# Kernel optimization log

Measured on AMD Instinct MI355X. Metric: run time of the kernel, lower is better.

Reference implementation:

```python
import jax, jax.numpy as jnp
import numpy as np
from jax import lax

D, C, H, W = 4, 64, 64, 64
QK = 32  # q/k projection channels


def _conv3x3(x, w, b):
    # x: [D,C,H,W], w: [O,I,3,3] -> [D,O,H,W], SAME padding, stride 1
    y = lax.conv_general_dilated(x, w, window_strides=(1, 1), padding='SAME',
                                 dimension_numbers=('NCHW', 'OIHW', 'NCHW'))
    return y + b[None, :, None, None]


def setup_inputs() -> dict:
    key = jax.random.key(0)
    ks = jax.random.split(key, 6)
    x = jax.random.normal(ks[0], (D, C, H, W), dtype=jnp.float32)
    atten = jax.random.normal(ks[1], (D, H * W, H * W), dtype=jnp.float32)
    q_w = jax.random.normal(ks[2], (QK, C, 3, 3), dtype=jnp.float32) * 0.05
    q_b = jax.random.normal(ks[3], (QK,), dtype=jnp.float32) * 0.05
    k_w = jax.random.normal(ks[4], (QK, C, 3, 3), dtype=jnp.float32) * 0.05
    k_b = jax.random.normal(ks[5], (QK,), dtype=jnp.float32) * 0.05
    gamma = jnp.ones((1,), dtype=jnp.float32)
    return {"x": x, "atten": atten, "q_w": q_w, "q_b": q_b,
            "k_w": k_w, "k_b": k_b, "gamma": gamma}


def reference(x, atten, q_w, q_b, k_w, k_b, gamma):
    d, c, h, w = x.shape
    n = h * w
    q = _conv3x3(x, q_w, q_b).reshape(d, QK, n)   # [D,32,N]
    k = _conv3x3(x, k_w, k_b).reshape(d, QK, n)   # [D,32,N]
    v = x.reshape(d, c, n)                         # [D,C,N]
    # attention = softmax(q^T k), then softmax(attention + atten) -- double softmax
    attn = jax.nn.softmax(jnp.einsum('dcn,dcm->dnm', q, k), axis=-1)  # [D,N,N]
    attn = jax.nn.softmax(attn + atten, axis=-1)
    # out = v @ attn^T  -> [D,C,N]
    out = jnp.einsum('dcm,dnm->dcn', v, attn).reshape(d, c, h, w)
    return gamma * out + x
```

## Files before the change

kernel.cpp:

```cpp
#include <hip/hip_runtime.h>
#include <hip/hip_bf16.h>

typedef float  f32x4  __attribute__((ext_vector_type(4)));
typedef float  f32x4u __attribute__((ext_vector_type(4), aligned(4)));
typedef short  s16x4  __attribute__((ext_vector_type(4)));
typedef short  s16x8  __attribute__((ext_vector_type(8)));
typedef __bf16 bf16x8 __attribute__((ext_vector_type(8)));

#define N_PIX 4096

__device__ __forceinline__ unsigned short f2bf(float f) {
    __hip_bfloat16 h = __float2bfloat16(f);
    return *reinterpret_cast<unsigned short*>(&h);
}
__device__ __forceinline__ float bf2f(unsigned short u) {
    __hip_bfloat16 h;
    *reinterpret_cast<unsigned short*>(&h) = u;
    return __bfloat162float(h);
}

#if __has_builtin(__builtin_amdgcn_mfma_f32_16x16x16bf16_1k)
#define USE_K16 1
#else
#define USE_K16 0
#endif

__device__ __forceinline__ f32x4 mac_k32v(s16x8 a8, s16x8 b8, f32x4 c) {
#if USE_K16
    s16x4 alo = __builtin_shufflevector(a8, a8, 0, 1, 2, 3);
    s16x4 ahi = __builtin_shufflevector(a8, a8, 4, 5, 6, 7);
    s16x4 blo = __builtin_shufflevector(b8, b8, 0, 1, 2, 3);
    s16x4 bhi = __builtin_shufflevector(b8, b8, 4, 5, 6, 7);
    c = __builtin_amdgcn_mfma_f32_16x16x16bf16_1k(alo, blo, c, 0, 0, 0);
    c = __builtin_amdgcn_mfma_f32_16x16x16bf16_1k(ahi, bhi, c, 0, 0, 0);
#else
    c = __builtin_amdgcn_mfma_f32_16x16x32_bf16(__builtin_bit_cast(bf16x8, a8),
                                                __builtin_bit_cast(bf16x8, b8), c, 0, 0, 0);
#endif
    return c;
}

__global__ __launch_bounds__(256) void to_bf16_kernel(const float* __restrict__ x,
                                                      unsigned short* __restrict__ v_bf) {
    int i = blockIdx.x * 256 + threadIdx.x;
    f32x4 f = *(const f32x4*)(x + i * 4);
    s16x4 p;
    p[0] = (short)f2bf(f[0]); p[1] = (short)f2bf(f[1]);
    p[2] = (short)f2bf(f[2]); p[3] = (short)f2bf(f[3]);
    *(s16x4*)(v_bf + i * 4) = p;
}

__global__ __launch_bounds__(256) void pad_kernel(const float* __restrict__ x,
                                                  float* __restrict__ xp) {
    int i = blockIdx.x * 256 + threadIdx.x;
    int xx = i % 66;
    int t  = i / 66;
    int yy = t % 66;
    int cd = t / 66;
    float v = 0.f;
    if (xx >= 1 && xx <= 64 && yy >= 1 && yy <= 64)
        v = x[(size_t)cd * 4096 + (yy - 1) * 64 + (xx - 1)];
    xp[i] = v;
}

__global__ __launch_bounds__(256) void conv_qk_kernel(
    const float* __restrict__ xp,
    const float* __restrict__ q_w, const float* __restrict__ q_b,
    const float* __restrict__ k_w, const float* __restrict__ k_b,
    unsigned short* __restrict__ qTp_hi, unsigned short* __restrict__ qTp_lo,
    unsigned short* __restrict__ kTp_hi, unsigned short* __restrict__ kTp_lo) {
    int bid = blockIdx.x;
    int d    = bid & 3;
    int rest = bid >> 2;
    int o  = __builtin_amdgcn_readfirstlane(rest & 31);
    int yg = rest >> 5;
    int tid = threadIdx.x;
    int y   = yg * 4 + (tid >> 6);
    int col = tid & 63;
    const float* xc0 = xp + (size_t)d * (64 * 4356) + y * 66 + col;
    const float* wq = q_w + o * 576;
    const float* wk = k_w + o * 576;
    float aq0 = 0.f, aq1 = 0.f, aq2 = 0.f, ak0 = 0.f, ak1 = 0.f, ak2 = 0.f;
#pragma unroll 4
    for (int c = 0; c < 64; ++c) {
        const float* xc = xc0 + c * 4356;
        f32x4u r0 = *(const f32x4u*)(xc);
        f32x4u r1 = *(const f32x4u*)(xc + 66);
        f32x4u r2 = *(const f32x4u*)(xc + 132);
        const float* wqc = wq + c * 9;
        const float* wkc = wk + c * 9;
        aq0 = fmaf(wqc[0], r0[0], fmaf(wqc[1], r0[1], fmaf(wqc[2], r0[2], aq0)));
        aq1 = fmaf(wqc[3], r1[0], fmaf(wqc[4], r1[1], fmaf(wqc[5], r1[2], aq1)));
        aq2 = fmaf(wqc[6], r2[0], fmaf(wqc[7], r2[1], fmaf(wqc[8], r2[2], aq2)));
        ak0 = fmaf(wkc[0], r0[0], fmaf(wkc[1], r0[1], fmaf(wkc[2], r0[2], ak0)));
        ak1 = fmaf(wkc[3], r1[0], fmaf(wkc[4], r1[1], fmaf(wkc[5], r1[2], ak1)));
        ak2 = fmaf(wkc[6], r2[0], fmaf(wkc[7], r2[1], fmaf(wkc[8], r2[2], ak2)));
    }
    float aq = aq0 + aq1 + aq2 + q_b[o];
    float ak = ak0 + ak1 + ak2 + k_b[o];
    int n = y * 64 + col;
    size_t base = ((size_t)d * N_PIX + n) * 32 + o;
    unsigned short qh = f2bf(aq);
    unsigned short ql = f2bf(aq - bf2f(qh));
    unsigned short kh = f2bf(ak);
    unsigned short kl = f2bf(ak - bf2f(kh));
    qTp_hi[base] = qh; qTp_lo[base] = ql;
    kTp_hi[base] = kh; kTp_lo[base] = kl;
}

__global__ __launch_bounds__(256) void attn_kernel(
    const float* __restrict__ x, const float* __restrict__ atten,
    const float* __restrict__ gamma,
    const unsigned short* __restrict__ qTp_hi, const unsigned short* __restrict__ qTp_lo,
    const unsigned short* __restrict__ kTp_hi, const unsigned short* __restrict__ kTp_lo,
    const unsigned short* __restrict__ v_bf, float* __restrict__ out) {
    __shared__ __align__(16) unsigned short P_s[4][2][16][72];
    __shared__ float Lred[4][16];
    __shared__ float Ared[4][64][17];

    int tid  = threadIdx.x;
    int lane = tid & 63;
    int w    = tid >> 6;
    int n16 = lane & 15;
    int g   = lane >> 4;
    int bid = blockIdx.x;
    int d   = bid & 3;
    int rb  = (bid >> 2) << 4;
    int nrow = rb + n16;

    size_t qrow = ((size_t)d * N_PIX + nrow) * 32;
    s16x8 qh8 = *(const s16x8*)(qTp_hi + qrow + 8 * g);
    s16x8 ql8 = *(const s16x8*)(qTp_lo + qrow + 8 * g);

    const unsigned short* kTh_d = kTp_hi + (size_t)d * N_PIX * 32;
    const unsigned short* kTl_d = kTp_lo + (size_t)d * N_PIX * 32;

    float l1p = 0.f;
    for (int i = 0; i < 16; ++i) {
        int m0 = (i * 4 + w) * 64;
        s16x8 kh8[4], kl8[4];
#pragma unroll
        for (int t = 0; t < 4; ++t) {
            size_t krow = (size_t)(m0 + t * 16 + n16) * 32;
            kh8[t] = *(const s16x8*)(kTh_d + krow + 8 * g);
            kl8[t] = *(const s16x8*)(kTl_d + krow + 8 * g);
        }
#pragma unroll
        for (int t = 0; t < 4; ++t) {
            f32x4 s = {0.f, 0.f, 0.f, 0.f};
            s = mac_k32v(kh8[t], qh8, s);
            s = mac_k32v(kh8[t], ql8, s);
            s = mac_k32v(kl8[t], qh8, s);
            l1p += __expf(s[0] - 40.f) + __expf(s[1] - 40.f) +
                   __expf(s[2] - 40.f) + __expf(s[3] - 40.f);
        }
    }
    l1p += __shfl_xor(l1p, 16, 64);
    l1p += __shfl_xor(l1p, 32, 64);
    if (g == 0) Lred[w][n16] = l1p;
    __syncthreads();
    float L1 = Lred[0][n16] + Lred[1][n16] + Lred[2][n16] + Lred[3][n16];
    float rcpL1 = 1.f / L1;

    const float* arow = atten + ((size_t)d << 24) + (size_t)nrow * N_PIX;
    const unsigned short* v_d = v_bf + (size_t)d * 64 * N_PIX;
    float l2p = 0.f;
    f32x4 acco[4];
#pragma unroll
    for (int ct = 0; ct < 4; ++ct) acco[ct] = f32x4{0.f, 0.f, 0.f, 0.f};

    for (int i = 0; i < 16; ++i) {
        int m0 = (i * 4 + w) * 64;
        int buf = i & 1;
        f32x4 av4[4];
#pragma unroll
        for (int t = 0; t < 4; ++t)
            av4[t] = *(const f32x4*)&arow[m0 + t * 16 + 4 * g];
        s16x8 kh8[4], kl8[4];
#pragma unroll
        for (int t = 0; t < 4; ++t) {
            size_t krow = (size_t)(m0 + t * 16 + n16) * 32;
            kh8[t] = *(const s16x8*)(kTh_d + krow + 8 * g);
            kl8[t] = *(const s16x8*)(kTl_d + krow + 8 * g);
        }
#pragma unroll
        for (int t = 0; t < 4; ++t) {
            f32x4 s = {0.f, 0.f, 0.f, 0.f};
            s = mac_k32v(kh8[t], qh8, s);
            s = mac_k32v(kh8[t], ql8, s);
            s = mac_k32v(kl8[t], qh8, s);
            s16x4 pp;
#pragma unroll
            for (int r = 0; r < 4; ++r) {
                float attn1 = __expf(s[r] - 40.f) * rcpL1;
                float p = __expf(attn1 + av4[t][r] - 8.f);
                l2p += p;
                pp[r] = (short)f2bf(p);
            }
            *(s16x4*)&P_s[w][buf][n16][t * 16 + 4 * g] = pp;
        }
        asm volatile("" ::: "memory");

#pragma unroll
        for (int h = 0; h < 2; ++h) {
            s16x8 p8 = *(const s16x8*)&P_s[w][buf][n16][h * 32 + 8 * g];
#pragma unroll
            for (int ct = 0; ct < 4; ++ct) {
                const unsigned short* vr = v_d + (size_t)(ct * 16 + n16) * N_PIX + m0 + h * 32;
                s16x8 v8 = *(const s16x8*)(vr + 8 * g);
                acco[ct] = mac_k32v(v8, p8, acco[ct]);
            }
        }
    }

    __syncthreads();
    l2p += __shfl_xor(l2p, 16, 64);
    l2p += __shfl_xor(l2p, 32, 64);
    if (g == 0) Lred[w][n16] = l2p;
#pragma unroll
    for (int ct = 0; ct < 4; ++ct)
#pragma unroll
        for (int r = 0; r < 4; ++r)
            Ared[w][lane][ct * 4 + r] = acco[ct][r];
    __syncthreads();

    if (w == 0) {
        float L2 = Lred[0][n16] + Lred[1][n16] + Lred[2][n16] + Lred[3][n16];
        float rcpL2 = 1.f / L2;
        float gam = gamma[0];
#pragma unroll
        for (int ct = 0; ct < 4; ++ct) {
#pragma unroll
            for (int r = 0; r < 4; ++r) {
                int j = ct * 4 + r;
                float tot = Ared[0][lane][j] + Ared[1][lane][j] +
                            Ared[2][lane][j] + Ared[3][lane][j];
                int c = ct * 16 + 4 * g + r;
                size_t idx = ((size_t)(d * 64 + c)) * N_PIX + rb + n16;
                out[idx] = gam * tot * rcpL2 + x[idx];
            }
        }
    }
}

extern "C" void kernel_launch(void* const* d_in, const int* in_sizes, int n_in,
                              void* d_out, int out_size, void* d_ws, size_t ws_size,
                              hipStream_t stream) {
    const float* x     = (const float*)d_in[0];
    const float* atten = (const float*)d_in[1];
    const float* q_w   = (const float*)d_in[2];
    const float* q_b   = (const float*)d_in[3];
    const float* k_w   = (const float*)d_in[4];
    const float* k_b   = (const float*)d_in[5];
    const float* gamma = (const float*)d_in[6];
    float* out = (float*)d_out;

    char* ws = (char*)d_ws;
    const size_t MB = 1u << 20;
    unsigned short* qTp_hi = (unsigned short*)(ws + 0 * MB);
    unsigned short* qTp_lo = (unsigned short*)(ws + 1 * MB);
    unsigned short* kTp_hi = (unsigned short*)(ws + 2 * MB);
    unsigned short* kTp_lo = (unsigned short*)(ws + 3 * MB);
    unsigned short* v_bf   = (unsigned short*)(ws + 4 * MB);
    float*          xp     = (float*)(ws + 8 * MB);

    hipLaunchKernelGGL(to_bf16_kernel, dim3(1024), dim3(256), 0, stream, x, v_bf);
    hipLaunchKernelGGL(pad_kernel, dim3(4356), dim3(256), 0, stream, x, xp);
    hipLaunchKernelGGL(conv_qk_kernel, dim3(2048), dim3(256), 0, stream,
                       xp, q_w, q_b, k_w, k_b, qTp_hi, qTp_lo, kTp_hi, kTp_lo);
    hipLaunchKernelGGL(attn_kernel, dim3(1024), dim3(256), 0, stream,
                       x, atten, gamma, qTp_hi, qTp_lo, kTp_hi, kTp_lo, v_bf, out);
}
```

Measured before the change: 530.8 us.

## Stream atten tiles into LDS with double-buffered global_load_lds and swizzled layout

Replaces the per-lane direct global loads of the `atten` matrix with cooperative `global_load_lds` transfers into a double-buffered, XOR-swizzled LDS tile. The next tile is prefetched while the current one is consumed, and the first tile is issued before the L1 reduction. The P staging buffer is also swizzled, drops its double buffer, and shares a unioned shared-memory region, with occupancy raised via launch bounds. The added per-iteration barrier and vmcnt(0) wait serialize the waves, which could offset the gain from better-coalesced, overlapped atten reads.

```diff
diff --git a/kernel.cpp b/kernel.cpp
--- a/kernel.cpp
+++ b/kernel.cpp
@@ -17,6 +17,13 @@
     __hip_bfloat16 h;
     *reinterpret_cast<unsigned short*>(&h) = u;
     return __bfloat162float(h);
+}
+
+__device__ __forceinline__ void gload_lds16(const void* g, void* l) {
+    __builtin_amdgcn_global_load_lds(
+        (const __attribute__((address_space(1))) unsigned int*)g,
+        (__attribute__((address_space(3))) unsigned int*)l,
+        16, 0, 0);
 }
 
 #if __has_builtin(__builtin_amdgcn_mfma_f32_16x16x16bf16_1k)
@@ -108,24 +115,26 @@
     kTp_hi[base] = kh; kTp_lo[base] = kl;
 }
 
-__global__ __launch_bounds__(256) void attn_kernel(
+__global__ __launch_bounds__(256, 4) void attn_kernel(
     const float* __restrict__ x, const float* __restrict__ atten,
     const float* __restrict__ gamma,
     const unsigned short* __restrict__ qTp_hi, const unsigned short* __restrict__ qTp_lo,
     const unsigned short* __restrict__ kTp_hi, const unsigned short* __restrict__ kTp_lo,
     const unsigned short* __restrict__ v_bf, float* __restrict__ out) {
-    __shared__ __align__(16) unsigned short P_s[4][2][16][72];
-    __shared__ float Lred[4][16];
-    __shared__ float Ared[4][64][17];
+    __shared__ __align__(16) char smem[40960];
+    float (*tile)[16][256]       = (float (*)[16][256])smem;
+    unsigned short (*P_s)[16][64] = (unsigned short (*)[16][64])(smem + 32768);
+    float (*Lred)[16]            = (float (*)[16])(smem + 32768);
+    float (*Ared)[64][17]        = (float (*)[64][17])smem;
 
     int tid  = threadIdx.x;
     int lane = tid & 63;
     int w    = tid >> 6;
-    int n16 = lane & 15;
-    int g   = lane >> 4;
-    int bid = blockIdx.x;
-    int d   = bid & 3;
-    int rb  = (bid >> 2) << 4;
+    int n16  = lane & 15;
+    int g    = lane >> 4;
+    int bid  = blockIdx.x;
+    int d    = bid & 3;
+    int rb   = (bid >> 2) << 4;
     int nrow = rb + n16;
 
     size_t qrow = ((size_t)d * N_PIX + nrow) * 32;
@@ -134,6 +143,7 @@
 
     const unsigned short* kTh_d = kTp_hi + (size_t)d * N_PIX * 32;
     const unsigned short* kTl_d = kTp_lo + (size_t)d * N_PIX * 32;
+    const float* atten_d = atten + ((size_t)d << 24);
 
     float l1p = 0.f;
     for (int i = 0; i < 16; ++i) {
@@ -155,14 +165,18 @@
                    __expf(s[2] - 40.f) + __expf(s[3] - 40.f);
         }
     }
+#pragma unroll
+    for (int j = 0; j < 4; ++j) {
+        int r = 4 * w + j;
+        const float* gp = atten_d + (size_t)(rb + r) * N_PIX + ((lane ^ (r & 7)) << 2);
+        gload_lds16(gp, (void*)&tile[0][r][0]);
+    }
     l1p += __shfl_xor(l1p, 16, 64);
     l1p += __shfl_xor(l1p, 32, 64);
     if (g == 0) Lred[w][n16] = l1p;
     __syncthreads();
-    float L1 = Lred[0][n16] + Lred[1][n16] + Lred[2][n16] + Lred[3][n16];
-    float rcpL1 = 1.f / L1;
-
-    const float* arow = atten + ((size_t)d << 24) + (size_t)nrow * N_PIX;
+    float rcpL1 = 1.f / (Lred[0][n16] + Lred[1][n16] + Lred[2][n16] + Lred[3][n16]);
+
     const unsigned short* v_d = v_bf + (size_t)d * 64 * N_PIX;
     float l2p = 0.f;
     f32x4 acco[4];
@@ -171,11 +185,6 @@
 
     for (int i = 0; i < 16; ++i) {
         int m0 = (i * 4 + w) * 64;
-        int buf = i & 1;
-        f32x4 av4[4];
-#pragma unroll
-        for (int t = 0; t < 4; ++t)
-            av4[t] = *(const f32x4*)&arow[m0 + t * 16 + 4 * g];
         s16x8 kh8[4], kl8[4];
 #pragma unroll
         for (int t = 0; t < 4; ++t) {
@@ -183,27 +192,47 @@
             kh8[t] = *(const s16x8*)(kTh_d + krow + 8 * g);
             kl8[t] = *(const s16x8*)(kTl_d + krow + 8 * g);
         }
+        f32x4 sArr[4];
 #pragma unroll
         for (int t = 0; t < 4; ++t) {
             f32x4 s = {0.f, 0.f, 0.f, 0.f};
             s = mac_k32v(kh8[t], qh8, s);
             s = mac_k32v(kh8[t], ql8, s);
             s = mac_k32v(kl8[t], qh8, s);
+            sArr[t] = s;
+        }
+        asm volatile("s_waitcnt vmcnt(0)" ::: "memory");
+        __builtin_amdgcn_s_barrier();
+        if (i < 15) {
+#pragma unroll
+            for (int j = 0; j < 4; ++j) {
+                int r = 4 * w + j;
+                const float* gp = atten_d + (size_t)(rb + r) * N_PIX + (i + 1) * 256 +
+                                  ((lane ^ (r & 7)) << 2);
+                gload_lds16(gp, (void*)&tile[(i + 1) & 1][r][0]);
+            }
+        }
+        const char* trow = (const char*)&tile[i & 1][n16][0];
+        char* prow = (char*)&P_s[w][n16][0];
+#pragma unroll
+        for (int t = 0; t < 4; ++t) {
+            int chunk = 16 * w + 4 * t + g;
+            f32x4 av = *(const f32x4*)(trow + ((chunk ^ (n16 & 7)) << 4));
             s16x4 pp;
 #pragma unroll
             for (int r = 0; r < 4; ++r) {
-                float attn1 = __expf(s[r] - 40.f) * rcpL1;
-                float p = __expf(attn1 + av4[t][r] - 8.f);
+                float attn1 = __expf(sArr[t][r] - 40.f) * rcpL1;
+                float p = __expf(attn1 + av[r] - 8.f);
                 l2p += p;
                 pp[r] = (short)f2bf(p);
             }
-            *(s16x4*)&P_s[w][buf][n16][t * 16 + 4 * g] = pp;
+            *(s16x4*)(prow + ((t * 32 + 8 * g) ^ ((n16 & 7) << 4))) = pp;
         }
         asm volatile("" ::: "memory");
 
 #pragma unroll
         for (int h = 0; h < 2; ++h) {
-            s16x8 p8 = *(const s16x8*)&P_s[w][buf][n16][h * 32 + 8 * g];
+            s16x8 p8 = *(const s16x8*)(prow + ((h * 64 + 16 * g) ^ ((n16 & 7) << 4)));
 #pragma unroll
             for (int ct = 0; ct < 4; ++ct) {
                 const unsigned short* vr = v_d + (size_t)(ct * 16 + n16) * N_PIX + m0 + h * 32;
@@ -211,11 +240,12 @@
                 acco[ct] = mac_k32v(v8, p8, acco[ct]);
             }
         }
-    }
-
-    __syncthreads();
+        asm volatile("" ::: "memory");
+    }
+
     l2p += __shfl_xor(l2p, 16, 64);
     l2p += __shfl_xor(l2p, 32, 64);
+    __syncthreads();
     if (g == 0) Lred[w][n16] = l2p;
 #pragma unroll
     for (int ct = 0; ct < 4; ++ct)
```

Measured after the change: 500.7 us. 1.06x faster.
